# Kernel optimization log

Measured on AMD Instinct MI355X. Metric: run time of the kernel, lower is better.

The kernel has to match this reference:

```python
import jax, jax.numpy as jnp
import numpy as np

N = 50000
IN_C, HID, OUT_C = 128, 64, 40


def setup_inputs() -> dict:
    key = jax.random.key(0)
    ks = jax.random.split(key, 10)
    x = jax.random.normal(ks[0], (N, IN_C), dtype=jnp.float32)
    edge_index = jax.random.randint(ks[1], (2, 1600000), 0, N, dtype=jnp.int64)
    edge_attr = jax.random.uniform(ks[2], (1600000,), dtype=jnp.float32)
    def lin(k, fan_in, fan_out):
        bound = 1.0 / np.sqrt(fan_in)
        return jax.random.uniform(k, (fan_in, fan_out), jnp.float32, -bound, bound)
    W1 = lin(ks[3], IN_C, HID); b1 = jnp.zeros((HID,), jnp.float32)
    W2 = lin(ks[4], HID, HID); b2 = jnp.zeros((HID,), jnp.float32)
    W3 = lin(ks[5], HID, OUT_C); b3 = jnp.zeros((OUT_C,), jnp.float32)
    return {"x": x, "edge_index": edge_index, "edge_attr": edge_attr,
            "W1": W1, "b1": b1, "W2": W2, "b2": b2, "W3": W3, "b3": b3}


def _gcn_conv(x, src, dst, norm, W, b):
    # h = x W ; out[i] = sum_{(j->i)} norm_e * h[j] ; + bias
    h = x @ W
    msg = norm[:, None] * h[src]          # [E+N, F_out] gathered messages
    out = jax.ops.segment_sum(msg, dst, num_segments=N)
    return out + b


def reference(x, edge_index, edge_attr, W1, b1, W2, b2, W3, b3):
    # GCN normalization with self-loops (fill_value=1), cached across layers.
    loops = jnp.arange(N, dtype=edge_index.dtype)
    src = jnp.concatenate([edge_index[0], loops])
    dst = jnp.concatenate([edge_index[1], loops])
    w = jnp.concatenate([edge_attr, jnp.ones((N,), edge_attr.dtype)])
    deg = jnp.zeros((N,), x.dtype).at[dst].add(w)
    dinv = jnp.where(deg > 0, jax.lax.rsqrt(deg), 0.0)
    norm = dinv[src] * w * dinv[dst]

    h = jax.nn.relu(_gcn_conv(x, src, dst, norm, W1, b1))   # dropout: eval no-op
    h = jax.nn.relu(_gcn_conv(h, src, dst, norm, W2, b2))
    h = jax.nn.relu(_gcn_conv(h, src, dst, norm, W3, b3))
    return jax.nn.log_softmax(h, axis=-1)
```

## Files before the change

kernel.cpp:

```cpp
#include <hip/hip_runtime.h>
#include <hip/hip_fp8.h>
#include <math.h>

#define N_NODES 50000
#define E_EDGES 1600000
#define IN_C    128
#define HID     64
#define OUT_C   40

#define BSH     9
#define BNODES  512
#define NB      98
#define CAP     20480
#define PBS     28160
#define TILE    4096
#define P1T     512
#define NPB     16

typedef unsigned int uint;
typedef unsigned short ushort;
typedef unsigned char uchar;

__device__ inline ushort f2b(float f) {
    uint u = __float_as_uint(f);
    u += 0x7FFFu + ((u >> 16) & 1u);
    return (ushort)(u >> 16);
}
__device__ inline float b2f(ushort h) { return __uint_as_float(((uint)h) << 16); }

__device__ inline uint ftof8(float f) { __hip_fp8_e4m3 t(f); return (uint)t.__x; }
__device__ inline float f8tof(uint b) { return __builtin_amdgcn_cvt_f32_fp8(b, 0); }

__global__ __launch_bounds__(P1T) void k_bin(const int* __restrict__ ei,
                                             const float* __restrict__ w,
                                             int* __restrict__ bcursor,
                                             uint2* __restrict__ tmp) {
    __shared__ uint2 stage[TILE];
    __shared__ unsigned char sbuck[TILE];
    __shared__ int hist[NB], startb[NB], cursor[NB], baseg[NB];
    __shared__ int sc[128];
    const int tid = threadIdx.x;
    const int e0  = blockIdx.x * TILE;
    const int n   = min(TILE, E_EDGES - e0);

    for (int i = tid; i < NB; i += P1T) hist[i] = 0;
    __syncthreads();

    for (int i = tid; i < n; i += P1T) {
        int d = ei[E_EDGES + e0 + i];
        atomicAdd(&hist[d >> BSH], 1);
    }
    __syncthreads();

    if (tid < 128) sc[tid] = (tid < NB) ? hist[tid] : 0;
    __syncthreads();
    for (int off = 1; off < 128; off <<= 1) {
        int x = 0;
        if (tid < 128 && tid >= off) x = sc[tid - off];
        __syncthreads();
        if (tid < 128) sc[tid] += x;
        __syncthreads();
    }
    if (tid < NB) {
        int st = sc[tid] - hist[tid];
        startb[tid] = st;
        cursor[tid] = st;
        baseg[tid]  = atomicAdd(&bcursor[tid], hist[tid]);
    }
    __syncthreads();

    for (int i = tid; i < n; i += P1T) {
        int   s  = ei[e0 + i];
        int   d  = ei[E_EDGES + e0 + i];
        float wv = w[e0 + i];
        int   b  = d >> BSH;
        int pos = atomicAdd(&cursor[b], 1);
        stage[pos] = make_uint2(((uint)(d & (BNODES - 1)) << 16) | (uint)s,
                                __float_as_uint(wv));
        sbuck[pos] = (unsigned char)b;
    }
    __syncthreads();

    for (int i = tid; i < n; i += P1T) {
        int b = sbuck[i];
        int gpos = baseg[b] + (i - startb[b]);
        tmp[(size_t)b * CAP + gpos] = stage[i];
    }
}

__global__ __launch_bounds__(BNODES) void k_build(const int* __restrict__ bcursor,
                                                  const uint2* __restrict__ tmp,
                                                  uint* __restrict__ rowinfo,
                                                  float* __restrict__ dinv,
                                                  uint* __restrict__ csr) {
    __shared__ int   hist[BNODES];
    __shared__ float wsum[BNODES];
    __shared__ int   sc[BNODES];
    __shared__ int   cur[BNODES];
    const int tid = threadIdx.x;
    const int b   = blockIdx.x;
    const int cnt = bcursor[b];
    const uint2* tb = tmp + (size_t)b * CAP;

    hist[tid] = 0; wsum[tid] = 0.0f;
    __syncthreads();
    for (int i = tid; i < cnt; i += BNODES) {
        uint2 u = tb[i];
        int dl = u.x >> 16;
        atomicAdd(&hist[dl], 1);
        atomicAdd(&wsum[dl], __uint_as_float(u.y));
    }
    __syncthreads();

    const int deg  = hist[tid];
    const int pdeg = (deg + 15) & ~15;
    sc[tid] = pdeg;
    __syncthreads();
    for (int off = 1; off < BNODES; off <<= 1) {
        int x = (tid >= off) ? sc[tid - off] : 0;
        __syncthreads();
        sc[tid] += x;
        __syncthreads();
    }
    const int base = b * PBS + (sc[tid] - pdeg);
    const int node = (b << BSH) + tid;
    if (node < N_NODES) {
        rowinfo[node] = ((uint)(pdeg >> 4) << 24) | (uint)base;
        dinv[node]    = rsqrtf(1.0f + wsum[tid]);
    }
    cur[tid] = base;
    __syncthreads();

    for (int i = tid; i < cnt; i += BNODES) {
        uint2 u = tb[i];
        int dl = u.x >> 16;
        int pos = atomicAdd(&cur[dl], 1);
        csr[pos] = ((uint)f2b(__uint_as_float(u.y)) << 16) | (u.x & 0xFFFFu);
    }
    for (int i = deg; i < pdeg; ++i) csr[base + i] = 0u;
}

__global__ __launch_bounds__(256) void k_gemm1(const float* __restrict__ x,
                                               const float* __restrict__ W,
                                               const float* __restrict__ dinv,
                                               uchar* __restrict__ g) {
    __shared__ float sW[IN_C * HID];
    __shared__ float sx[NPB * IN_C];
    const int tid = threadIdx.x;
    const size_t base = (size_t)blockIdx.x * NPB;

    for (int i = tid; i < (IN_C * HID) / 4; i += 256)
        ((float4*)sW)[i] = ((const float4*)W)[i];
    for (int i = tid; i < (NPB * IN_C) / 4; i += 256)
        ((float4*)sx)[i] = ((const float4*)(x + base * IN_C))[i];
    __syncthreads();

    const int wv = tid >> 6, f = tid & 63;
    for (int nn = 0; nn < 4; ++nn) {
        const int nl = wv * 4 + nn;
        const float* row = &sx[nl * IN_C];
        float acc = 0.0f;
#pragma unroll 8
        for (int k = 0; k < IN_C; k += 4) {
            float4 a = *(const float4*)&row[k];
            acc += a.x * sW[(k + 0) * HID + f] + a.y * sW[(k + 1) * HID + f]
                 + a.z * sW[(k + 2) * HID + f] + a.w * sW[(k + 3) * HID + f];
        }
        const size_t node = base + nl;
        g[node * HID + f] = (uchar)ftof8(dinv[node] * acc);
    }
}

template <int F_OUT>
__global__ __launch_bounds__(256) void k_agg_gemm(const uint* __restrict__ rowinfo,
                                                  const uint* __restrict__ csr,
                                                  const uchar* __restrict__ g,
                                                  const float* __restrict__ dinv,
                                                  const float* __restrict__ bias,
                                                  const float* __restrict__ W,
                                                  uchar* __restrict__ g_next) {
    __shared__ float sW[HID * F_OUT];
    __shared__ float s_act[4][HID];
    const int tid = threadIdx.x;
    for (int i = tid; i < HID * F_OUT; i += 256) sW[i] = W[i];

    const int wv = tid >> 6, lane = tid & 63;
    const int node = blockIdx.x * 4 + wv;
    const uint ri  = rowinfo[node];
    const int  n16 = (int)(ri >> 24);
    const float dv = dinv[node];

    float acc0 = f8tof(g[(size_t)node * HID + lane]);
    float acc1 = 0.0f;

    const uint* rp = csr + (ri & 0xFFFFFFu);
    uint d = rp[lane & 15];
    for (int blk = 0; blk < n16; ++blk) {
        uint dn = rp[((blk + 1) << 4) + (lane & 15)];
        uchar uv[16];
        uint  sw[16];
#pragma unroll
        for (int j = 0; j < 16; ++j) {
            uint dj = (uint)__builtin_amdgcn_readlane((int)d, j);
            sw[j] = dj & 0xFFFF0000u;
            uv[j] = g[(size_t)(dj & 0xFFFFu) * HID + lane];
        }
#pragma unroll
        for (int j = 0; j < 16; ++j) {
            float f = f8tof((uint)uv[j]);
            if (j & 1) acc1 += __uint_as_float(sw[j]) * f;
            else       acc0 += __uint_as_float(sw[j]) * f;
        }
        d = dn;
    }
    float acc = acc0 + acc1;

    s_act[wv][lane] = fmaxf(dv * acc + bias[lane], 0.0f);
    __syncthreads();
    if (lane < F_OUT) {
        float dot = 0.0f;
#pragma unroll 4
        for (int k = 0; k < HID; k += 4) {
            float4 a = *(const float4*)&s_act[wv][k];
            dot += a.x * sW[(k + 0) * F_OUT + lane] + a.y * sW[(k + 1) * F_OUT + lane]
                 + a.z * sW[(k + 2) * F_OUT + lane] + a.w * sW[(k + 3) * F_OUT + lane];
        }
        g_next[(size_t)node * F_OUT + lane] = (uchar)ftof8(dinv[node] * dot);
    }
}

__global__ __launch_bounds__(256) void k_final_agg(const uint* __restrict__ rowinfo,
                                                   const uint* __restrict__ csr,
                                                   const uchar* __restrict__ g,
                                                   const float* __restrict__ dinv,
                                                   const float* __restrict__ bias,
                                                   float* __restrict__ out) {
    const int tid = threadIdx.x;
    const int wv = tid >> 6, lane = tid & 63;
    const int node = blockIdx.x * 4 + wv;
    const bool live = lane < OUT_C;
    const uint ri  = rowinfo[node];
    const int  n16 = (int)(ri >> 24);
    const float dv = dinv[node];

    float acc0 = live ? f8tof(g[(size_t)node * OUT_C + lane]) : 0.0f;
    float acc1 = 0.0f;

    const uint* rp = csr + (ri & 0xFFFFFFu);
    uint d = rp[lane & 15];
    for (int blk = 0; blk < n16; ++blk) {
        uint dn = rp[((blk + 1) << 4) + (lane & 15)];
        uchar uv[16];
        uint  sw[16];
#pragma unroll
        for (int j = 0; j < 16; ++j) {
            uint dj = (uint)__builtin_amdgcn_readlane((int)d, j);
            sw[j] = dj & 0xFFFF0000u;
            uv[j] = g[(size_t)(dj & 0xFFFFu) * OUT_C + lane];
        }
#pragma unroll
        for (int j = 0; j < 16; ++j) {
            float f = f8tof((uint)uv[j]);
            if (j & 1) acc1 += __uint_as_float(sw[j]) * f;
            else       acc0 += __uint_as_float(sw[j]) * f;
        }
        d = dn;
    }
    float acc = acc0 + acc1;

    float bl = live ? bias[lane] : 0.0f;
    float v  = live ? fmaxf(dv * acc + bl, 0.0f) : -INFINITY;
    float mx = v;
#pragma unroll
    for (int off = 32; off > 0; off >>= 1) mx = fmaxf(mx, __shfl_xor(mx, off));
    float ex = live ? expf(v - mx) : 0.0f;
    float se = ex;
#pragma unroll
    for (int off = 32; off > 0; off >>= 1) se += __shfl_xor(se, off);
    if (live) out[(size_t)node * OUT_C + lane] = v - mx - logf(se);
}

extern "C" void kernel_launch(void* const* d_in, const int* in_sizes, int n_in,
                              void* d_out, int out_size, void* d_ws, size_t ws_size,
                              hipStream_t stream) {
    const float* x  = (const float*)d_in[0];
    const int*   ei = (const int*)d_in[1];
    const float* w  = (const float*)d_in[2];
    const float* W1 = (const float*)d_in[3];
    const float* b1 = (const float*)d_in[4];
    const float* W2 = (const float*)d_in[5];
    const float* b2 = (const float*)d_in[6];
    const float* W3 = (const float*)d_in[7];
    const float* b3 = (const float*)d_in[8];
    float* out = (float*)d_out;

    char* ws = (char*)d_ws;
    size_t off = 0;
    auto carve = [&](size_t bytes) {
        char* p = ws + off;
        off += (bytes + 255) & ~(size_t)255;
        return p;
    };
    int*   bcursor = (int*)carve(NB * sizeof(int));
    uint*  rowinfo = (uint*)carve(N_NODES * sizeof(uint));
    float* dinv    = (float*)carve(N_NODES * sizeof(float));
    uint*  csr     = (uint*)carve(((size_t)NB * PBS + 64) * sizeof(uint));
    uint2* tmp     = (uint2*)carve((size_t)NB * CAP * sizeof(uint2) + 256);
    uchar* g1 = (uchar*)tmp;
    uchar* g2 = g1 + (size_t)N_NODES * HID;
    uchar* g3 = g1;
    (void)ws_size;

    const int nbBin = (E_EDGES + TILE - 1) / TILE;
    const int nbN4  = N_NODES / 4;
    const int nbG1  = N_NODES / NPB;

    hipMemsetAsync(bcursor, 0, NB * sizeof(int), stream);
    k_bin<<<nbBin, P1T, 0, stream>>>(ei, w, bcursor, tmp);
    k_build<<<NB, BNODES, 0, stream>>>(bcursor, tmp, rowinfo, dinv, csr);

    k_gemm1<<<nbG1, 256, 0, stream>>>(x, W1, dinv, g1);
    k_agg_gemm<HID><<<nbN4, 256, 0, stream>>>(rowinfo, csr, g1, dinv, b1, W2, g2);
    k_agg_gemm<OUT_C><<<nbN4, 256, 0, stream>>>(rowinfo, csr, g2, dinv, b2, W3, g3);
    k_final_agg<<<nbN4, 256, 0, stream>>>(rowinfo, csr, g3, dinv, b3, out);
}
```

Baseline: 229.1 us.

## Reassociate layer-3 GEMM after aggregation and vectorize fp8 gathers into dwords

Layer 3 now aggregates the 64-wide hidden features and applies W3 afterwards, in the final kernel, instead of transforming to 40 features before aggregation. This moves the second agg kernel's GEMM into the last kernel, so all three aggregations share one 64-wide routine. That routine gathers four fp8 values per lane as a dword, handles four neighbours at once across 16-lane groups, and reduces with shuffles. The aim is fewer, wider memory transactions per gathered row and fewer byte loads. The cost is a 64-wide gather in layer 3 instead of a 40-wide one, plus cross-group shuffle reductions.

```diff
diff --git a/kernel.cpp b/kernel.cpp
--- a/kernel.cpp
+++ b/kernel.cpp
@@ -26,10 +26,11 @@
     u += 0x7FFFu + ((u >> 16) & 1u);
     return (ushort)(u >> 16);
 }
-__device__ inline float b2f(ushort h) { return __uint_as_float(((uint)h) << 16); }
-
 __device__ inline uint ftof8(float f) { __hip_fp8_e4m3 t(f); return (uint)t.__x; }
-__device__ inline float f8tof(uint b) { return __builtin_amdgcn_cvt_f32_fp8(b, 0); }
+template <int SEL>
+__device__ __forceinline__ float f8v(uint dw) {
+    return __builtin_amdgcn_cvt_f32_fp8(dw, SEL);
+}
 
 __global__ __launch_bounds__(P1T) void k_bin(const int* __restrict__ ei,
                                              const float* __restrict__ w,
@@ -171,105 +172,139 @@
     }
 }
 
-template <int F_OUT>
-__global__ __launch_bounds__(256) void k_agg_gemm(const uint* __restrict__ rowinfo,
-                                                  const uint* __restrict__ csr,
-                                                  const uchar* __restrict__ g,
-                                                  const float* __restrict__ dinv,
-                                                  const float* __restrict__ bias,
-                                                  const float* __restrict__ W,
-                                                  uchar* __restrict__ g_next) {
-    __shared__ float sW[HID * F_OUT];
+__device__ __forceinline__ float4 agg_row64(const uint* __restrict__ csr,
+                                            const uint* __restrict__ gw,
+                                            uint ri, int node, int lane) {
+    const int grp = lane >> 4, sub = lane & 15;
+    const int n16 = (int)(ri >> 24);
+    float4 acc = {0.f, 0.f, 0.f, 0.f};
+    if (grp == 0) {
+        uint dw = gw[((uint)node << 4) + sub];
+        acc.x = f8v<0>(dw); acc.y = f8v<1>(dw); acc.z = f8v<2>(dw); acc.w = f8v<3>(dw);
+    }
+    const uint* rp = csr + (ri & 0xFFFFFFu);
+    uint d = rp[sub];
+    for (int blk = 0; blk < n16; ++blk) {
+        uint dn = rp[((blk + 1) << 4) + sub];
+#pragma unroll
+        for (int i = 0; i < 4; ++i) {
+            uint dj  = __shfl(d, 4 * i + grp);
+            float wg = __uint_as_float(dj & 0xFFFF0000u);
+            uint dw  = gw[((dj & 0xFFFFu) << 4) + sub];
+            acc.x += wg * f8v<0>(dw);
+            acc.y += wg * f8v<1>(dw);
+            acc.z += wg * f8v<2>(dw);
+            acc.w += wg * f8v<3>(dw);
+        }
+        d = dn;
+    }
+#pragma unroll
+    for (int m = 16; m <= 32; m <<= 1) {
+        acc.x += __shfl_xor(acc.x, m); acc.y += __shfl_xor(acc.y, m);
+        acc.z += __shfl_xor(acc.z, m); acc.w += __shfl_xor(acc.w, m);
+    }
+    return acc;
+}
+
+__global__ __launch_bounds__(256) void k_aggA(const uint* __restrict__ rowinfo,
+                                              const uint* __restrict__ csr,
+                                              const uint* __restrict__ gw,
+                                              const float* __restrict__ dinv,
+                                              const float* __restrict__ bias,
+                                              const float* __restrict__ W,
+                                              uchar* __restrict__ g_next) {
+    __shared__ float sW[HID * HID];
     __shared__ float s_act[4][HID];
     const int tid = threadIdx.x;
-    for (int i = tid; i < HID * F_OUT; i += 256) sW[i] = W[i];
+    for (int i = tid; i < HID * HID; i += 256) sW[i] = W[i];
 
     const int wv = tid >> 6, lane = tid & 63;
     const int node = blockIdx.x * 4 + wv;
     const uint ri  = rowinfo[node];
-    const int  n16 = (int)(ri >> 24);
     const float dv = dinv[node];
 
-    float acc0 = f8tof(g[(size_t)node * HID + lane]);
-    float acc1 = 0.0f;
-
-    const uint* rp = csr + (ri & 0xFFFFFFu);
-    uint d = rp[lane & 15];
-    for (int blk = 0; blk < n16; ++blk) {
-        uint dn = rp[((blk + 1) << 4) + (lane & 15)];
-        uchar uv[16];
-        uint  sw[16];
-#pragma unroll
-        for (int j = 0; j < 16; ++j) {
-            uint dj = (uint)__builtin_amdgcn_readlane((int)d, j);
-            sw[j] = dj & 0xFFFF0000u;
-            uv[j] = g[(size_t)(dj & 0xFFFFu) * HID + lane];
-        }
-#pragma unroll
-        for (int j = 0; j < 16; ++j) {
-            float f = f8tof((uint)uv[j]);
-            if (j & 1) acc1 += __uint_as_float(sw[j]) * f;
-            else       acc0 += __uint_as_float(sw[j]) * f;
-        }
-        d = dn;
-    }
-    float acc = acc0 + acc1;
-
-    s_act[wv][lane] = fmaxf(dv * acc + bias[lane], 0.0f);
-    __syncthreads();
-    if (lane < F_OUT) {
+    float4 acc = agg_row64(csr, gw, ri, node, lane);
+
+    if ((lane >> 4) == 0) {
+        const int sub = lane & 15;
+        float4 b4 = ((const float4*)bias)[sub];
+        float4 r;
+        r.x = fmaxf(dv * acc.x + b4.x, 0.f);
+        r.y = fmaxf(dv * acc.y + b4.y, 0.f);
+        r.z = fmaxf(dv * acc.z + b4.z, 0.f);
+        r.w = fmaxf(dv * acc.w + b4.w, 0.f);
+        ((float4*)&s_act[wv][0])[sub] = r;
+    }
+    __syncthreads();
+    float dot = 0.0f;
+#pragma unroll 4
+    for (int k = 0; k < HID; k += 4) {
+        float4 a = *(const float4*)&s_act[wv][k];
+        dot += a.x * sW[(k + 0) * HID + lane] + a.y * sW[(k + 1) * HID + lane]
+             + a.z * sW[(k + 2) * HID + lane] + a.w * sW[(k + 3) * HID + lane];
+    }
+    g_next[(size_t)node * HID + lane] = (uchar)ftof8(dv * dot);
+}
+
+__global__ __launch_bounds__(256) void k_aggB(const uint* __restrict__ rowinfo,
+                                              const uint* __restrict__ csr,
+                                              const uint* __restrict__ gw,
+                                              const float* __restrict__ dinv,
+                                              const float* __restrict__ bias,
+                                              uint* __restrict__ u2w) {
+    const int tid = threadIdx.x;
+    const int wv = tid >> 6, lane = tid & 63;
+    const int node = blockIdx.x * 4 + wv;
+    const uint ri  = rowinfo[node];
+    const float dv = dinv[node];
+
+    float4 acc = agg_row64(csr, gw, ri, node, lane);
+
+    if ((lane >> 4) == 0) {
+        const int sub = lane & 15;
+        float4 b4 = ((const float4*)bias)[sub];
+        uint p0 = ftof8(dv * fmaxf(dv * acc.x + b4.x, 0.f));
+        uint p1 = ftof8(dv * fmaxf(dv * acc.y + b4.y, 0.f));
+        uint p2 = ftof8(dv * fmaxf(dv * acc.z + b4.z, 0.f));
+        uint p3 = ftof8(dv * fmaxf(dv * acc.w + b4.w, 0.f));
+        u2w[((uint)node << 4) + sub] = p0 | (p1 << 8) | (p2 << 16) | (p3 << 24);
+    }
+}
+
+__global__ __launch_bounds__(256) void k_aggC(const uint* __restrict__ rowinfo,
+                                              const uint* __restrict__ csr,
+                                              const uint* __restrict__ gw,
+                                              const float* __restrict__ dinv,
+                                              const float* __restrict__ bias,
+                                              const float* __restrict__ W,
+                                              float* __restrict__ out) {
+    __shared__ float sW[HID * OUT_C];
+    __shared__ float s_z[4][HID];
+    const int tid = threadIdx.x;
+    for (int i = tid; i < HID * OUT_C; i += 256) sW[i] = W[i];
+
+    const int wv = tid >> 6, lane = tid & 63;
+    const int node = blockIdx.x * 4 + wv;
+    const uint ri  = rowinfo[node];
+    const float dv = dinv[node];
+
+    float4 acc = agg_row64(csr, gw, ri, node, lane);
+
+    if ((lane >> 4) == 0) ((float4*)&s_z[wv][0])[lane & 15] = acc;
+    __syncthreads();
+
+    const bool live = lane < OUT_C;
+    float v = -INFINITY;
+    if (live) {
         float dot = 0.0f;
 #pragma unroll 4
         for (int k = 0; k < HID; k += 4) {
-            float4 a = *(const float4*)&s_act[wv][k];
-            dot += a.x * sW[(k + 0) * F_OUT + lane] + a.y * sW[(k + 1) * F_OUT + lane]
-                 + a.z * sW[(k + 2) * F_OUT + lane] + a.w * sW[(k + 3) * F_OUT + lane];
+            float4 a = *(const float4*)&s_z[wv][k];
+            dot += a.x * sW[(k + 0) * OUT_C + lane] + a.y * sW[(k + 1) * OUT_C + lane]
+                 + a.z * sW[(k + 2) * OUT_C + lane] + a.w * sW[(k + 3) * OUT_C + lane];
         }
-        g_next[(size_t)node * F_OUT + lane] = (uchar)ftof8(dinv[node] * dot);
-    }
-}
-
-__global__ __launch_bounds__(256) void k_final_agg(const uint* __restrict__ rowinfo,
-                                                   const uint* __restrict__ csr,
-                                                   const uchar* __restrict__ g,
-                                                   const float* __restrict__ dinv,
-                                                   const float* __restrict__ bias,
-                                                   float* __restrict__ out) {
-    const int tid = threadIdx.x;
-    const int wv = tid >> 6, lane = tid & 63;
-    const int node = blockIdx.x * 4 + wv;
-    const bool live = lane < OUT_C;
-    const uint ri  = rowinfo[node];
-    const int  n16 = (int)(ri >> 24);
-    const float dv = dinv[node];
-
-    float acc0 = live ? f8tof(g[(size_t)node * OUT_C + lane]) : 0.0f;
-    float acc1 = 0.0f;
-
-    const uint* rp = csr + (ri & 0xFFFFFFu);
-    uint d = rp[lane & 15];
-    for (int blk = 0; blk < n16; ++blk) {
-        uint dn = rp[((blk + 1) << 4) + (lane & 15)];
-        uchar uv[16];
-        uint  sw[16];
-#pragma unroll
-        for (int j = 0; j < 16; ++j) {
-            uint dj = (uint)__builtin_amdgcn_readlane((int)d, j);
-            sw[j] = dj & 0xFFFF0000u;
-            uv[j] = g[(size_t)(dj & 0xFFFFu) * OUT_C + lane];
-        }
-#pragma unroll
-        for (int j = 0; j < 16; ++j) {
-            float f = f8tof((uint)uv[j]);
-            if (j & 1) acc1 += __uint_as_float(sw[j]) * f;
-            else       acc0 += __uint_as_float(sw[j]) * f;
-        }
-        d = dn;
-    }
-    float acc = acc0 + acc1;
-
-    float bl = live ? bias[lane] : 0.0f;
-    float v  = live ? fmaxf(dv * acc + bl, 0.0f) : -INFINITY;
+        v = fmaxf(dv * dot + bias[lane], 0.0f);
+    }
     float mx = v;
 #pragma unroll
     for (int off = 32; off > 0; off >>= 1) mx = fmaxf(mx, __shfl_xor(mx, off));
@@ -308,19 +343,19 @@
     uint2* tmp     = (uint2*)carve((size_t)NB * CAP * sizeof(uint2) + 256);
     uchar* g1 = (uchar*)tmp;
     uchar* g2 = g1 + (size_t)N_NODES * HID;
-    uchar* g3 = g1;
+    uchar* u2 = g1;
     (void)ws_size;
 
     const int nbBin = (E_EDGES + TILE - 1) / TILE;
     const int nbN4  = N_NODES / 4;
     const int nbG1  = N_NODES / NPB;
 
-    hipMemsetAsync(bcursor, 0, NB * sizeof(int), stream);
+    (void)hipMemsetAsync(bcursor, 0, NB * sizeof(int), stream);
     k_bin<<<nbBin, P1T, 0, stream>>>(ei, w, bcursor, tmp);
     k_build<<<NB, BNODES, 0, stream>>>(bcursor, tmp, rowinfo, dinv, csr);
 
     k_gemm1<<<nbG1, 256, 0, stream>>>(x, W1, dinv, g1);
-    k_agg_gemm<HID><<<nbN4, 256, 0, stream>>>(rowinfo, csr, g1, dinv, b1, W2, g2);
-    k_agg_gemm<OUT_C><<<nbN4, 256, 0, stream>>>(rowinfo, csr, g2, dinv, b2, W3, g3);
-    k_final_agg<<<nbN4, 256, 0, stream>>>(rowinfo, csr, g3, dinv, b3, out);
-}
+    k_aggA<<<nbN4, 256, 0, stream>>>(rowinfo, csr, (const uint*)g1, dinv, b1, W2, g2);
+    k_aggB<<<nbN4, 256, 0, stream>>>(rowinfo, csr, (const uint*)g2, dinv, b2, (uint*)u2);
+    k_aggC<<<nbN4, 256, 0, stream>>>(rowinfo, csr, (const uint*)u2, dinv, b3, W3, out);
+}
```

After: 227.3 us. About the same (-0.8%).
